# Performance work log

Measured on AMD Instinct MI355X. Metric: run time of the kernel, lower is better.

Reference implementation:

```python
import jax, jax.numpy as jnp
import numpy as np

TEMPERATURE = 8.0  # sqrt(d_head=64)

def setup_inputs() -> dict:
    key = jax.random.key(0)
    kq, kk, kv = jax.random.split(key, 3)
    B, S, D = 4, 4096, 64
    Q = jax.random.normal(kq, (B, S, D), dtype=jnp.float32)
    K = jax.random.normal(kk, (B, S, D), dtype=jnp.float32)
    V = jax.random.normal(kv, (B, S, D), dtype=jnp.float32)
    return {"Q": Q, "K": K, "V": V}

def reference(Q, K, V):
    # attn_scores = Q @ K^T / temperature  -> [B, S, S]
    scores = jnp.einsum('bqd,bkd->bqk', Q, K) / TEMPERATURE
    weights = jax.nn.softmax(scores, axis=-1)
    # NOTE: original module multiplies weights by K (not V) -- faithful to source.
    out = jnp.einsum('bqk,bkd->bqd', weights, K)
    return out
```

## Files before the change

### kernel.cpp

```cpp
#include <hip/hip_runtime.h>
#include <hip/hip_bf16.h>


#define SQ   4096
#define DH   64
#define NB   4
#define QBLK 128
#define KBLK 32

typedef __bf16 bf16x8 __attribute__((ext_vector_type(8)));
typedef float  f32x16 __attribute__((ext_vector_type(16)));
typedef unsigned int u32x4 __attribute__((ext_vector_type(4)));

struct Buf {
  unsigned short Ks[KBLK][72];
  unsigned short Kt[DH][36];
};

__device__ __forceinline__ unsigned short f2bf(float f) {
  return __builtin_bit_cast(unsigned short, (__bf16)f);
}
__device__ __forceinline__ float bf2f(unsigned short u) {
  return __builtin_bit_cast(float, (unsigned int)u << 16);
}

template <int NS, bool FINAL>
__global__ __launch_bounds__(256, 4)
void attn_fwd(const float* __restrict__ Qg, const float* __restrict__ Kg,
              float* __restrict__ Og, unsigned short* __restrict__ Uws,
              float* __restrict__ Lws) {
  __shared__ Buf lds[3];
  const int tid  = threadIdx.x;
  const int lane = tid & 63;
  const int c32  = lane & 31;
  const int h    = lane >> 5;

  constexpr int QT = SQ / QBLK;
  const int split = blockIdx.x / (NB * QT);
  const int rem   = blockIdx.x % (NB * QT);
  const int batch = rem / QT;
  const int qt    = rem % QT;
  const int q0w   = qt * QBLK + (tid >> 6) * 32;
  constexpr int NT = (SQ / NS) / KBLK;

  const float cf = 0.18033688011112042f;
  bf16x8 qf[4];
  {
    const float* qrow = Qg + ((size_t)(batch * SQ + q0w + c32)) * DH + 8 * h;
#pragma unroll
    for (int dc = 0; dc < 4; ++dc) {
      const float4 a = *(const float4*)(qrow + dc * 16);
      const float4 b = *(const float4*)(qrow + dc * 16 + 4);
      bf16x8 t;
      t[0] = (__bf16)(a.x * cf); t[1] = (__bf16)(a.y * cf);
      t[2] = (__bf16)(a.z * cf); t[3] = (__bf16)(a.w * cf);
      t[4] = (__bf16)(b.x * cf); t[5] = (__bf16)(b.y * cf);
      t[6] = (__bf16)(b.z * cf); t[7] = (__bf16)(b.w * cf);
      qf[dc] = t;
    }
  }

  f32x16 acc0 = {};
  f32x16 acc1 = {};
  float l = 0.f;

  const float* kbase =
      Kg + (size_t)batch * SQ * DH + (size_t)split * (SQ / NS) * DH;
  const int row0 = (tid >> 4) * 2;
  const int col0 = (tid & 15) * 4;

  float4 f0, f1;
  auto loadv = [&](int t) {
    const float* p = kbase + ((size_t)t * KBLK + row0) * DH + col0;
    f0 = *(const float4*)(p);
    f1 = *(const float4*)(p + DH);
  };
  auto stage = [&](int b) {
    const ushort4 u0 = make_ushort4(f2bf(f0.x), f2bf(f0.y), f2bf(f0.z), f2bf(f0.w));
    const ushort4 u1 = make_ushort4(f2bf(f1.x), f2bf(f1.y), f2bf(f1.z), f2bf(f1.w));
    *(ushort4*)&lds[b].Ks[row0][col0]     = u0;
    *(ushort4*)&lds[b].Ks[row0 + 1][col0] = u1;
    *(unsigned int*)&lds[b].Kt[col0 + 0][row0] = (unsigned)u0.x | ((unsigned)u1.x << 16);
    *(unsigned int*)&lds[b].Kt[col0 + 1][row0] = (unsigned)u0.y | ((unsigned)u1.y << 16);
    *(unsigned int*)&lds[b].Kt[col0 + 2][row0] = (unsigned)u0.z | ((unsigned)u1.z << 16);
    *(unsigned int*)&lds[b].Kt[col0 + 3][row0] = (unsigned)u0.w | ((unsigned)u1.w << 16);
  };
  auto qkt = [&](int b) {
    f32x16 s = {};
#pragma unroll
    for (int dc = 0; dc < 4; ++dc) {
      bf16x8 kf = *(const bf16x8*)&lds[b].Ks[c32][dc * 16 + 8 * h];
      s = __builtin_amdgcn_mfma_f32_32x32x16_bf16(kf, qf[dc], s, 0, 0, 0);
    }
    return s;
  };
  auto smpv = [&](f32x16 sv, int b) {
    float ts = 0.f;
#pragma unroll
    for (int r = 0; r < 16; ++r) { sv[r] = exp2f(sv[r]); ts += sv[r]; }
    l += ts;

    unsigned int dw[8];
#pragma unroll
    for (int d = 0; d < 8; ++d)
      asm("v_cvt_pk_bf16_f32 %0, %1, %2"
          : "=v"(dw[d]) : "v"(sv[2 * d]), "v"(sv[2 * d + 1]));
    asm("v_permlane32_swap_b32 %0, %1" : "+v"(dw[0]), "+v"(dw[2]));
    asm("v_permlane32_swap_b32 %0, %1" : "+v"(dw[1]), "+v"(dw[3]));
    asm("v_permlane32_swap_b32 %0, %1" : "+v"(dw[4]), "+v"(dw[6]));
    asm("v_permlane32_swap_b32 %0, %1" : "+v"(dw[5]), "+v"(dw[7]));
    u32x4 w0 = {dw[0], dw[1], dw[2], dw[3]};
    u32x4 w1 = {dw[4], dw[5], dw[6], dw[7]};
    const bf16x8 pb0 = __builtin_bit_cast(bf16x8, w0);
    const bf16x8 pb1 = __builtin_bit_cast(bf16x8, w1);

    bf16x8 t00 = *(const bf16x8*)&lds[b].Kt[c32][8 * h];
    bf16x8 t01 = *(const bf16x8*)&lds[b].Kt[c32][16 + 8 * h];
    bf16x8 t10 = *(const bf16x8*)&lds[b].Kt[32 + c32][8 * h];
    bf16x8 t11 = *(const bf16x8*)&lds[b].Kt[32 + c32][16 + 8 * h];
    acc0 = __builtin_amdgcn_mfma_f32_32x32x16_bf16(t00, pb0, acc0, 0, 0, 0);
    acc0 = __builtin_amdgcn_mfma_f32_32x32x16_bf16(t01, pb1, acc0, 0, 0, 0);
    acc1 = __builtin_amdgcn_mfma_f32_32x32x16_bf16(t10, pb0, acc1, 0, 0, 0);
    acc1 = __builtin_amdgcn_mfma_f32_32x32x16_bf16(t11, pb1, acc1, 0, 0, 0);
  };

  loadv(0);
  stage(0);
  loadv(1);
  __syncthreads();
  f32x16 s = qkt(0);

  int bc = 0, bn = 1;
  for (int t = 0; t < NT - 1; ++t) {
    stage(bn);
    if (t + 2 < NT) loadv(t + 2);
    __syncthreads();
    f32x16 n = qkt(bn);
    smpv(s, bc);
    s = n;
    bc = bn;
    bn = (bn == 2) ? 0 : bn + 1;
  }
  smpv(s, bc);

  l += __shfl_xor(l, 32);

  if (FINAL) {
    const float scale = 1.0f / l;
    float* orow = Og + ((size_t)(batch * SQ) + q0w + c32) * DH;
#pragma unroll
    for (int mm = 0; mm < 4; ++mm) {
      float4 w0 = make_float4(acc0[4 * mm] * scale, acc0[4 * mm + 1] * scale,
                              acc0[4 * mm + 2] * scale, acc0[4 * mm + 3] * scale);
      float4 w1 = make_float4(acc1[4 * mm] * scale, acc1[4 * mm + 1] * scale,
                              acc1[4 * mm + 2] * scale, acc1[4 * mm + 3] * scale);
      *(float4*)(orow + 8 * mm + 4 * h)      = w0;
      *(float4*)(orow + 32 + 8 * mm + 4 * h) = w1;
    }
  } else {
    unsigned short* urow =
        Uws + ((size_t)((split * NB + batch) * SQ) + q0w + c32) * DH;
#pragma unroll
    for (int mm = 0; mm < 4; ++mm) {
      *(ushort4*)(urow + 8 * mm + 4 * h) =
          make_ushort4(f2bf(acc0[4 * mm]), f2bf(acc0[4 * mm + 1]),
                       f2bf(acc0[4 * mm + 2]), f2bf(acc0[4 * mm + 3]));
      *(ushort4*)(urow + 32 + 8 * mm + 4 * h) =
          make_ushort4(f2bf(acc1[4 * mm]), f2bf(acc1[4 * mm + 1]),
                       f2bf(acc1[4 * mm + 2]), f2bf(acc1[4 * mm + 3]));
    }
    if (h == 0)
      Lws[(size_t)(split * NB + batch) * SQ + q0w + c32] = l;
  }
}

template <int NS>
__global__ __launch_bounds__(256, 4)
void combine_splits(const unsigned short* __restrict__ U,
                    const float* __restrict__ L, float* __restrict__ O) {
  const int idx = blockIdx.x * 256 + threadIdx.x;
  const int row = idx >> 4;
  const int d4  = (idx & 15) << 2;
  const int RT  = NB * SQ;

  float den = 0.f;
#pragma unroll
  for (int i = 0; i < NS; ++i) den += L[(size_t)i * RT + row];
  const float rden = 1.0f / den;

  float4 o = make_float4(0.f, 0.f, 0.f, 0.f);
#pragma unroll
  for (int i = 0; i < NS; ++i) {
    const ushort4 u = *(const ushort4*)&U[((size_t)i * RT + row) * DH + d4];
    o.x += bf2f(u.x); o.y += bf2f(u.y); o.z += bf2f(u.z); o.w += bf2f(u.w);
  }
  o.x *= rden; o.y *= rden; o.z *= rden; o.w *= rden;
  *(float4*)&O[(size_t)row * DH + d4] = o;
}

extern "C" void kernel_launch(void* const* d_in, const int* in_sizes, int n_in,
                              void* d_out, int out_size, void* d_ws, size_t ws_size,
                              hipStream_t stream) {
  const float* Q = (const float*)d_in[0];
  const float* K = (const float*)d_in[1];
  float* O = (float*)d_out;

  auto need = [](int ns) {
    return (size_t)ns * NB * SQ * DH * 2 + (size_t)ns * NB * SQ * 4;
  };

  if (ws_size >= need(8)) {
    constexpr int NS = 8;
    unsigned short* U = (unsigned short*)d_ws;
    float* L = (float*)(U + (size_t)NS * NB * SQ * DH);
    attn_fwd<NS, false><<<dim3(NS * NB * (SQ / QBLK)), 256, 0, stream>>>(Q, K, nullptr, U, L);
    combine_splits<NS><<<dim3((NB * SQ * 16) / 256), 256, 0, stream>>>(U, L, O);
  } else if (ws_size >= need(4)) {
    constexpr int NS = 4;
    unsigned short* U = (unsigned short*)d_ws;
    float* L = (float*)(U + (size_t)NS * NB * SQ * DH);
    attn_fwd<NS, false><<<dim3(NS * NB * (SQ / QBLK)), 256, 0, stream>>>(Q, K, nullptr, U, L);
    combine_splits<NS><<<dim3((NB * SQ * 16) / 256), 256, 0, stream>>>(U, L, O);
  } else {
    attn_fwd<1, true><<<dim3(NB * (SQ / QBLK)), 256, 0, stream>>>(Q, K, O, nullptr, nullptr);
  }
}
```

Measured before the change: 42.44 us.

## Process two 32-row query tiles per wave to reuse K fragments

Each wave now handles 64 query rows as two 32-row tiles sharing the same LDS K and K-transpose fragments, doubling the MFMA work per LDS read. The Q block grows to 256 rows, the software-pipelined QK^T/PV overlap is replaced by a straight per-tile loop, and the split count is raised to 16 so the grid stays large. This cuts LDS traffic and K staging per query, at the cost of more registers (launch bounds lowered to 3 waves), lost cross-iteration overlap, and a larger workspace and combine pass.

```diff
diff --git a/kernel.cpp b/kernel.cpp
--- a/kernel.cpp
+++ b/kernel.cpp
@@ -5,7 +5,7 @@
 #define SQ   4096
 #define DH   64
 #define NB   4
-#define QBLK 128
+#define QBLK 256
 #define KBLK 32
 
 typedef __bf16 bf16x8 __attribute__((ext_vector_type(8)));
@@ -25,7 +25,7 @@
 }
 
 template <int NS, bool FINAL>
-__global__ __launch_bounds__(256, 4)
+__global__ __launch_bounds__(256, 3)
 void attn_fwd(const float* __restrict__ Qg, const float* __restrict__ Kg,
               float* __restrict__ Og, unsigned short* __restrict__ Uws,
               float* __restrict__ Lws) {
@@ -40,29 +40,38 @@
   const int rem   = blockIdx.x % (NB * QT);
   const int batch = rem / QT;
   const int qt    = rem % QT;
-  const int q0w   = qt * QBLK + (tid >> 6) * 32;
+  const int q0w   = qt * QBLK + (tid >> 6) * 64;
   constexpr int NT = (SQ / NS) / KBLK;
 
   const float cf = 0.18033688011112042f;
-  bf16x8 qf[4];
+  bf16x8 qfA[4], qfB[4];
   {
-    const float* qrow = Qg + ((size_t)(batch * SQ + q0w + c32)) * DH + 8 * h;
+    const float* qrowA = Qg + ((size_t)(batch * SQ + q0w + c32)) * DH + 8 * h;
+    const float* qrowB = qrowA + (size_t)32 * DH;
 #pragma unroll
     for (int dc = 0; dc < 4; ++dc) {
-      const float4 a = *(const float4*)(qrow + dc * 16);
-      const float4 b = *(const float4*)(qrow + dc * 16 + 4);
+      const float4 a = *(const float4*)(qrowA + dc * 16);
+      const float4 b = *(const float4*)(qrowA + dc * 16 + 4);
       bf16x8 t;
       t[0] = (__bf16)(a.x * cf); t[1] = (__bf16)(a.y * cf);
       t[2] = (__bf16)(a.z * cf); t[3] = (__bf16)(a.w * cf);
       t[4] = (__bf16)(b.x * cf); t[5] = (__bf16)(b.y * cf);
       t[6] = (__bf16)(b.z * cf); t[7] = (__bf16)(b.w * cf);
-      qf[dc] = t;
-    }
-  }
-
-  f32x16 acc0 = {};
-  f32x16 acc1 = {};
-  float l = 0.f;
+      qfA[dc] = t;
+      const float4 c = *(const float4*)(qrowB + dc * 16);
+      const float4 d = *(const float4*)(qrowB + dc * 16 + 4);
+      bf16x8 u;
+      u[0] = (__bf16)(c.x * cf); u[1] = (__bf16)(c.y * cf);
+      u[2] = (__bf16)(c.z * cf); u[3] = (__bf16)(c.w * cf);
+      u[4] = (__bf16)(d.x * cf); u[5] = (__bf16)(d.y * cf);
+      u[6] = (__bf16)(d.z * cf); u[7] = (__bf16)(d.w * cf);
+      qfB[dc] = u;
+    }
+  }
+
+  f32x16 acc0A = {}, acc1A = {};
+  f32x16 acc0B = {}, acc1B = {};
+  float lA = 0.f, lB = 0.f;
 
   const float* kbase =
       Kg + (size_t)batch * SQ * DH + (size_t)split * (SQ / NS) * DH;
@@ -85,21 +94,14 @@
     *(unsigned int*)&lds[b].Kt[col0 + 2][row0] = (unsigned)u0.z | ((unsigned)u1.z << 16);
     *(unsigned int*)&lds[b].Kt[col0 + 3][row0] = (unsigned)u0.w | ((unsigned)u1.w << 16);
   };
-  auto qkt = [&](int b) {
-    f32x16 s = {};
-#pragma unroll
-    for (int dc = 0; dc < 4; ++dc) {
-      bf16x8 kf = *(const bf16x8*)&lds[b].Ks[c32][dc * 16 + 8 * h];
-      s = __builtin_amdgcn_mfma_f32_32x32x16_bf16(kf, qf[dc], s, 0, 0, 0);
-    }
-    return s;
-  };
-  auto smpv = [&](f32x16 sv, int b) {
-    float ts = 0.f;
-#pragma unroll
-    for (int r = 0; r < 16; ++r) { sv[r] = exp2f(sv[r]); ts += sv[r]; }
-    l += ts;
-
+
+  auto smvalu = [&](f32x16 sv, float& lacc, bf16x8& pb0, bf16x8& pb1) {
+    float t0 = 0.f, t1 = 0.f;
+#pragma unroll
+    for (int r = 0; r < 8; ++r) { sv[r] = exp2f(sv[r]); t0 += sv[r]; }
+#pragma unroll
+    for (int r = 8; r < 16; ++r) { sv[r] = exp2f(sv[r]); t1 += sv[r]; }
+    lacc += t0 + t1;
     unsigned int dw[8];
 #pragma unroll
     for (int d = 0; d < 8; ++d)
@@ -111,66 +113,101 @@
     asm("v_permlane32_swap_b32 %0, %1" : "+v"(dw[5]), "+v"(dw[7]));
     u32x4 w0 = {dw[0], dw[1], dw[2], dw[3]};
     u32x4 w1 = {dw[4], dw[5], dw[6], dw[7]};
-    const bf16x8 pb0 = __builtin_bit_cast(bf16x8, w0);
-    const bf16x8 pb1 = __builtin_bit_cast(bf16x8, w1);
-
-    bf16x8 t00 = *(const bf16x8*)&lds[b].Kt[c32][8 * h];
-    bf16x8 t01 = *(const bf16x8*)&lds[b].Kt[c32][16 + 8 * h];
-    bf16x8 t10 = *(const bf16x8*)&lds[b].Kt[32 + c32][8 * h];
-    bf16x8 t11 = *(const bf16x8*)&lds[b].Kt[32 + c32][16 + 8 * h];
-    acc0 = __builtin_amdgcn_mfma_f32_32x32x16_bf16(t00, pb0, acc0, 0, 0, 0);
-    acc0 = __builtin_amdgcn_mfma_f32_32x32x16_bf16(t01, pb1, acc0, 0, 0, 0);
-    acc1 = __builtin_amdgcn_mfma_f32_32x32x16_bf16(t10, pb0, acc1, 0, 0, 0);
-    acc1 = __builtin_amdgcn_mfma_f32_32x32x16_bf16(t11, pb1, acc1, 0, 0, 0);
-  };
-
-  loadv(0);
-  stage(0);
+    pb0 = __builtin_bit_cast(bf16x8, w0);
+    pb1 = __builtin_bit_cast(bf16x8, w1);
+  };
+
+  loadv(0); stage(0);
   loadv(1);
   __syncthreads();
-  f32x16 s = qkt(0);
 
   int bc = 0, bn = 1;
-  for (int t = 0; t < NT - 1; ++t) {
-    stage(bn);
+  for (int t = 0; t < NT; ++t) {
+    if (t + 1 < NT) stage(bn);
     if (t + 2 < NT) loadv(t + 2);
     __syncthreads();
-    f32x16 n = qkt(bn);
-    smpv(s, bc);
-    s = n;
+
+    bf16x8 kf0 = *(const bf16x8*)&lds[bc].Ks[c32][0 * 16 + 8 * h];
+    bf16x8 kf1 = *(const bf16x8*)&lds[bc].Ks[c32][1 * 16 + 8 * h];
+    bf16x8 kf2 = *(const bf16x8*)&lds[bc].Ks[c32][2 * 16 + 8 * h];
+    bf16x8 kf3 = *(const bf16x8*)&lds[bc].Ks[c32][3 * 16 + 8 * h];
+    f32x16 sA = {}, sB = {};
+    sA = __builtin_amdgcn_mfma_f32_32x32x16_bf16(kf0, qfA[0], sA, 0, 0, 0);
+    sB = __builtin_amdgcn_mfma_f32_32x32x16_bf16(kf0, qfB[0], sB, 0, 0, 0);
+    sA = __builtin_amdgcn_mfma_f32_32x32x16_bf16(kf1, qfA[1], sA, 0, 0, 0);
+    sB = __builtin_amdgcn_mfma_f32_32x32x16_bf16(kf1, qfB[1], sB, 0, 0, 0);
+    sA = __builtin_amdgcn_mfma_f32_32x32x16_bf16(kf2, qfA[2], sA, 0, 0, 0);
+    sB = __builtin_amdgcn_mfma_f32_32x32x16_bf16(kf2, qfB[2], sB, 0, 0, 0);
+    sA = __builtin_amdgcn_mfma_f32_32x32x16_bf16(kf3, qfA[3], sA, 0, 0, 0);
+    sB = __builtin_amdgcn_mfma_f32_32x32x16_bf16(kf3, qfB[3], sB, 0, 0, 0);
+
+    bf16x8 tf0 = *(const bf16x8*)&lds[bc].Kt[c32][8 * h];
+    bf16x8 tf1 = *(const bf16x8*)&lds[bc].Kt[c32][16 + 8 * h];
+    bf16x8 tf2 = *(const bf16x8*)&lds[bc].Kt[32 + c32][8 * h];
+    bf16x8 tf3 = *(const bf16x8*)&lds[bc].Kt[32 + c32][16 + 8 * h];
+
+    bf16x8 pbA0, pbA1, pbB0, pbB1;
+    smvalu(sA, lA, pbA0, pbA1);
+    acc0A = __builtin_amdgcn_mfma_f32_32x32x16_bf16(tf0, pbA0, acc0A, 0, 0, 0);
+    acc0A = __builtin_amdgcn_mfma_f32_32x32x16_bf16(tf1, pbA1, acc0A, 0, 0, 0);
+    acc1A = __builtin_amdgcn_mfma_f32_32x32x16_bf16(tf2, pbA0, acc1A, 0, 0, 0);
+    acc1A = __builtin_amdgcn_mfma_f32_32x32x16_bf16(tf3, pbA1, acc1A, 0, 0, 0);
+    smvalu(sB, lB, pbB0, pbB1);
+    acc0B = __builtin_amdgcn_mfma_f32_32x32x16_bf16(tf0, pbB0, acc0B, 0, 0, 0);
+    acc0B = __builtin_amdgcn_mfma_f32_32x32x16_bf16(tf1, pbB1, acc0B, 0, 0, 0);
+    acc1B = __builtin_amdgcn_mfma_f32_32x32x16_bf16(tf2, pbB0, acc1B, 0, 0, 0);
+    acc1B = __builtin_amdgcn_mfma_f32_32x32x16_bf16(tf3, pbB1, acc1B, 0, 0, 0);
+
     bc = bn;
     bn = (bn == 2) ? 0 : bn + 1;
   }
-  smpv(s, bc);
-
-  l += __shfl_xor(l, 32);
+
+  lA += __shfl_xor(lA, 32);
+  lB += __shfl_xor(lB, 32);
 
   if (FINAL) {
-    const float scale = 1.0f / l;
-    float* orow = Og + ((size_t)(batch * SQ) + q0w + c32) * DH;
+    const float scA = 1.0f / lA, scB = 1.0f / lB;
+    float* orowA = Og + ((size_t)(batch * SQ) + q0w + c32) * DH;
+    float* orowB = orowA + (size_t)32 * DH;
 #pragma unroll
     for (int mm = 0; mm < 4; ++mm) {
-      float4 w0 = make_float4(acc0[4 * mm] * scale, acc0[4 * mm + 1] * scale,
-                              acc0[4 * mm + 2] * scale, acc0[4 * mm + 3] * scale);
-      float4 w1 = make_float4(acc1[4 * mm] * scale, acc1[4 * mm + 1] * scale,
-                              acc1[4 * mm + 2] * scale, acc1[4 * mm + 3] * scale);
-      *(float4*)(orow + 8 * mm + 4 * h)      = w0;
-      *(float4*)(orow + 32 + 8 * mm + 4 * h) = w1;
+      *(float4*)(orowA + 8 * mm + 4 * h) =
+          make_float4(acc0A[4 * mm] * scA, acc0A[4 * mm + 1] * scA,
+                      acc0A[4 * mm + 2] * scA, acc0A[4 * mm + 3] * scA);
+      *(float4*)(orowA + 32 + 8 * mm + 4 * h) =
+          make_float4(acc1A[4 * mm] * scA, acc1A[4 * mm + 1] * scA,
+                      acc1A[4 * mm + 2] * scA, acc1A[4 * mm + 3] * scA);
+      *(float4*)(orowB + 8 * mm + 4 * h) =
+          make_float4(acc0B[4 * mm] * scB, acc0B[4 * mm + 1] * scB,
+                      acc0B[4 * mm + 2] * scB, acc0B[4 * mm + 3] * scB);
+      *(float4*)(orowB + 32 + 8 * mm + 4 * h) =
+          make_float4(acc1B[4 * mm] * scB, acc1B[4 * mm + 1] * scB,
+                      acc1B[4 * mm + 2] * scB, acc1B[4 * mm + 3] * scB);
     }
   } else {
-    unsigned short* urow =
+    unsigned short* urowA =
         Uws + ((size_t)((split * NB + batch) * SQ) + q0w + c32) * DH;
+    unsigned short* urowB = urowA + (size_t)32 * DH;
 #pragma unroll
     for (int mm = 0; mm < 4; ++mm) {
-      *(ushort4*)(urow + 8 * mm + 4 * h) =
-          make_ushort4(f2bf(acc0[4 * mm]), f2bf(acc0[4 * mm + 1]),
-                       f2bf(acc0[4 * mm + 2]), f2bf(acc0[4 * mm + 3]));
-      *(ushort4*)(urow + 32 + 8 * mm + 4 * h) =
-          make_ushort4(f2bf(acc1[4 * mm]), f2bf(acc1[4 * mm + 1]),
-                       f2bf(acc1[4 * mm + 2]), f2bf(acc1[4 * mm + 3]));
-    }
-    if (h == 0)
-      Lws[(size_t)(split * NB + batch) * SQ + q0w + c32] = l;
+      *(ushort4*)(urowA + 8 * mm + 4 * h) =
+          make_ushort4(f2bf(acc0A[4 * mm]), f2bf(acc0A[4 * mm + 1]),
+                       f2bf(acc0A[4 * mm + 2]), f2bf(acc0A[4 * mm + 3]));
+      *(ushort4*)(urowA + 32 + 8 * mm + 4 * h) =
+          make_ushort4(f2bf(acc1A[4 * mm]), f2bf(acc1A[4 * mm + 1]),
+                       f2bf(acc1A[4 * mm + 2]), f2bf(acc1A[4 * mm + 3]));
+      *(ushort4*)(urowB + 8 * mm + 4 * h) =
+          make_ushort4(f2bf(acc0B[4 * mm]), f2bf(acc0B[4 * mm + 1]),
+                       f2bf(acc0B[4 * mm + 2]), f2bf(acc0B[4 * mm + 3]));
+      *(ushort4*)(urowB + 32 + 8 * mm + 4 * h) =
+          make_ushort4(f2bf(acc1B[4 * mm]), f2bf(acc1B[4 * mm + 1]),
+                       f2bf(acc1B[4 * mm + 2]), f2bf(acc1B[4 * mm + 3]));
+    }
+    if (h == 0) {
+      const size_t row = (size_t)(split * NB + batch) * SQ + q0w + c32;
+      Lws[row] = lA;
+      Lws[row + 32] = lB;
+    }
   }
 }
 
@@ -209,14 +246,14 @@
     return (size_t)ns * NB * SQ * DH * 2 + (size_t)ns * NB * SQ * 4;
   };
 
-  if (ws_size >= need(8)) {
-    constexpr int NS = 8;
+  if (ws_size >= need(16)) {
+    constexpr int NS = 16;
     unsigned short* U = (unsigned short*)d_ws;
     float* L = (float*)(U + (size_t)NS * NB * SQ * DH);
     attn_fwd<NS, false><<<dim3(NS * NB * (SQ / QBLK)), 256, 0, stream>>>(Q, K, nullptr, U, L);
     combine_splits<NS><<<dim3((NB * SQ * 16) / 256), 256, 0, stream>>>(U, L, O);
-  } else if (ws_size >= need(4)) {
-    constexpr int NS = 4;
+  } else if (ws_size >= need(8)) {
+    constexpr int NS = 8;
     unsigned short* U = (unsigned short*)d_ws;
     float* L = (float*)(U + (size_t)NS * NB * SQ * DH);
     attn_fwd<NS, false><<<dim3(NS * NB * (SQ / QBLK)), 256, 0, stream>>>(Q, K, nullptr, U, L);
```

Result: slower. 58.94 us (+38.9%).
